# Kernel optimization log

Hardware: AMD Instinct MI355X
Metric: run time of the kernel (lower is better)

The kernel has to match this reference:

```python
import jax, jax.numpy as jnp
import numpy as np

C = 128  # n_filters; input channels must equal n_filters due to residual


def setup_inputs() -> dict:
    key = jax.random.key(0)
    kx, kw = jax.random.split(key)
    x = jax.random.normal(kx, (8, 64, 512, C), dtype=jnp.float32)
    # 1x1 conv, no bias == dense over channel axis: [C, 2C]
    W_qkv = jax.random.normal(kw, (C, 2 * C), dtype=jnp.float32) * (1.0 / np.sqrt(C))
    return {"x": x, "W_qkv": W_qkv}


def reference(x, W_qkv):
    # qkv: [B,H,W,2C]; split -> qk [B,H,W,C] -> q,k [B,H,W,C/2]; v [B,H,W,C]
    qkv = jnp.einsum('bhwc,cd->bhwd', x, W_qkv)
    half = C // 2
    q = qkv[..., :half]
    k = qkv[..., half:C]
    v = qkv[..., C:]
    # scores over the W (time) axis; NOTE: original applies no 1/sqrt(d) scaling
    scores = jnp.einsum('bhqc,bhkc->bhqk', q, k)  # [B,H,W,W]
    w = jax.nn.softmax(scores, axis=-1)
    y = jnp.einsum('bhqk,bhkc->bhqc', w, v)  # [B,H,W,C]
    y = x + y  # with_skip_connection=True
    return (y, w)
```

## Files before the change

### kernel.cpp

```cpp
#include <hip/hip_runtime.h>
#include <hip/hip_bf16.h>

typedef short s16x8 __attribute__((ext_vector_type(8)));
typedef float f32x4 __attribute__((ext_vector_type(4)));

#define MFMA_BF16(a,b,c) __builtin_amdgcn_mfma_f32_16x16x32_bf16((a),(b),(c),0,0,0)

static __device__ __forceinline__ unsigned short f2bf(float f){
  unsigned u = __builtin_bit_cast(unsigned, f);
  u += 0x7fffu + ((u >> 16) & 1u);
  return (unsigned short)(u >> 16);
}
static __device__ __forceinline__ float bf2f(unsigned short h){
  unsigned u = ((unsigned)h) << 16;
  return __builtin_bit_cast(float, u);
}
static __device__ __forceinline__ int swzi(int row, int col, int lw){
  const int chunk = (col >> 3) ^ ((row ^ (row >> 3)) & 7);
  return row*lw + (chunk << 3) + (col & 7);
}

__global__ __launch_bounds__(128) void k0_wt(const float* __restrict__ W,
                                             unsigned short* __restrict__ wtH,
                                             unsigned short* __restrict__ wtL){
  const int n = blockIdx.x;
  const int c = threadIdx.x;
  const float v = W[(size_t)c*256 + n];
  const unsigned short h = f2bf(v);
  wtH[n*128 + c] = h;
  wtL[n*128 + c] = f2bf(v - bf2f(h));
}

__global__ __launch_bounds__(512,2) void k1_qkv(const float* __restrict__ x,
    const unsigned short* __restrict__ wtH, const unsigned short* __restrict__ wtL,
    unsigned short* __restrict__ qh, unsigned short* __restrict__ ql,
    unsigned short* __restrict__ kh, unsigned short* __restrict__ kl,
    unsigned short* __restrict__ vT){
  __shared__ unsigned short xh[16384], xl[16384];
  const int t = threadIdx.x;
  const int lane = t & 63, wid = t >> 6;
  const int li = lane & 15, g = lane >> 4;
  const int m0 = blockIdx.x * 128;
  const int wm = wid >> 2, wn = wid & 3;

  {
    const int row = t >> 2, cb = (t & 3) * 32;
    const float* src = x + (size_t)(m0 + row)*128 + cb;
    #pragma unroll
    for (int gg = 0; gg < 4; ++gg){
      const float4 v0 = ((const float4*)src)[2*gg];
      const float4 v1 = ((const float4*)src)[2*gg + 1];
      const float vv[8] = {v0.x,v0.y,v0.z,v0.w,v1.x,v1.y,v1.z,v1.w};
      s16x8 h, l;
      #pragma unroll
      for (int j = 0; j < 8; ++j){
        const unsigned short hb = f2bf(vv[j]);
        h[j] = (short)hb;
        l[j] = (short)f2bf(vv[j] - bf2f(hb));
      }
      const int idx = swzi(row, cb + 8*gg, 128);
      *(s16x8*)&xh[idx] = h;
      *(s16x8*)&xl[idx] = l;
    }
  }
  __syncthreads();

  {
    f32x4 acc[4][2] = {};
    #pragma unroll
    for (int ks = 0; ks < 4; ++ks){
      const int col = ks*32 + g*8;
      s16x8 ah[4], al[4];
      #pragma unroll
      for (int mi = 0; mi < 4; ++mi){
        const int idx = swzi(wm*64 + mi*16 + li, col, 128);
        ah[mi] = *(const s16x8*)&xh[idx];
        al[mi] = *(const s16x8*)&xl[idx];
      }
      #pragma unroll
      for (int ni = 0; ni < 2; ++ni){
        const size_t boff = (size_t)(wn*32 + ni*16 + li)*128 + col;
        const s16x8 bh = *(const s16x8*)(wtH + boff);
        const s16x8 bl = *(const s16x8*)(wtL + boff);
        #pragma unroll
        for (int mi = 0; mi < 4; ++mi){
          acc[mi][ni] = MFMA_BF16(bh, ah[mi], acc[mi][ni]);
          acc[mi][ni] = MFMA_BF16(bh, al[mi], acc[mi][ni]);
          acc[mi][ni] = MFMA_BF16(bl, ah[mi], acc[mi][ni]);
        }
      }
    }
    #pragma unroll
    for (int mi = 0; mi < 4; ++mi)
      #pragma unroll
      for (int ni = 0; ni < 2; ++ni){
        const int pos = m0 + wm*64 + mi*16 + li;
        const int och = wn*32 + ni*16 + g*4;
        ushort4 hv, lv;
        #pragma unroll
        for (int r = 0; r < 4; ++r){
          const float v = acc[mi][ni][r];
          const unsigned short hb = f2bf(v);
          ((unsigned short*)&hv)[r] = hb;
          ((unsigned short*)&lv)[r] = f2bf(v - bf2f(hb));
        }
        const size_t off = (size_t)pos*64 + (och & 63);
        if (wn < 2){ *(ushort4*)&qh[off] = hv; *(ushort4*)&ql[off] = lv; }
        else       { *(ushort4*)&kh[off] = hv; *(ushort4*)&kl[off] = lv; }
      }
  }

  {
    f32x4 acc[4][2] = {};
    #pragma unroll
    for (int ks = 0; ks < 4; ++ks){
      const int col = ks*32 + g*8;
      s16x8 ah[4], al[4];
      #pragma unroll
      for (int mi = 0; mi < 4; ++mi){
        const int idx = swzi(wm*64 + mi*16 + li, col, 128);
        ah[mi] = *(const s16x8*)&xh[idx];
        al[mi] = *(const s16x8*)&xl[idx];
      }
      #pragma unroll
      for (int ni = 0; ni < 2; ++ni){
        const size_t boff = (size_t)(128 + wn*32 + ni*16 + li)*128 + col;
        const s16x8 bh = *(const s16x8*)(wtH + boff);
        const s16x8 bl = *(const s16x8*)(wtL + boff);
        #pragma unroll
        for (int mi = 0; mi < 4; ++mi){
          acc[mi][ni] = MFMA_BF16(ah[mi], bh, acc[mi][ni]);
          acc[mi][ni] = MFMA_BF16(ah[mi], bl, acc[mi][ni]);
          acc[mi][ni] = MFMA_BF16(al[mi], bh, acc[mi][ni]);
        }
      }
    }
    #pragma unroll
    for (int mi = 0; mi < 4; ++mi)
      #pragma unroll
      for (int ni = 0; ni < 2; ++ni){
        const int growb = m0 + wm*64 + mi*16 + g*4;
        const int ch = wn*32 + ni*16 + li;
        const int head = growb >> 9, posb = growb & 511;
        ushort4 pv;
        #pragma unroll
        for (int r = 0; r < 4; ++r)
          ((unsigned short*)&pv)[r] = f2bf(acc[mi][ni][r]);
        *(ushort4*)&vT[((size_t)head << 16) + ch*512 + posb] = pv;
      }
  }
}

__global__ __launch_bounds__(256,4) void k2_attn(
    const unsigned short* __restrict__ qh, const unsigned short* __restrict__ ql,
    const unsigned short* __restrict__ kh, const unsigned short* __restrict__ kl,
    const unsigned short* __restrict__ vT, const float* __restrict__ x,
    float* __restrict__ y, float* __restrict__ wout){
  __shared__ unsigned short wlds[16384];
  __shared__ float redm[128], reds[128];

  const int t = threadIdx.x;
  const int lane = t & 63, wid = t >> 6;
  const int li = lane & 15, g = lane >> 4;
  const int bi = blockIdx.x;
  const int head = (bi & 7) + 8 * (bi >> 7);
  const int qt = (bi >> 3) & 15;
  const size_t hbase = (size_t)head * 512;
  const int q0 = qt * 32;
  const int kbase = wid * 128;

  f32x4 acc[2][8] = {};
  #pragma unroll
  for (int ks = 0; ks < 2; ++ks){
    const int col = ks*32 + g*8;
    s16x8 ah[2], al[2];
    #pragma unroll
    for (int mi = 0; mi < 2; ++mi){
      const size_t aoff = (hbase + q0 + mi*16 + li)*64 + col;
      ah[mi] = *(const s16x8*)(qh + aoff);
      al[mi] = *(const s16x8*)(ql + aoff);
    }
    #pragma unroll
    for (int ni = 0; ni < 8; ++ni){
      const size_t boff = (hbase + kbase + ni*16 + li)*64 + col;
      const s16x8 bh = *(const s16x8*)(kh + boff);
      const s16x8 bl = *(const s16x8*)(kl + boff);
      #pragma unroll
      for (int mi = 0; mi < 2; ++mi){
        acc[mi][ni] = MFMA_BF16(ah[mi], bh, acc[mi][ni]);
        acc[mi][ni] = MFMA_BF16(ah[mi], bl, acc[mi][ni]);
        acc[mi][ni] = MFMA_BF16(al[mi], bh, acc[mi][ni]);
      }
    }
  }

  #pragma unroll
  for (int mi = 0; mi < 2; ++mi)
    #pragma unroll
    for (int r = 0; r < 4; ++r){
      float m = acc[mi][0][r];
      #pragma unroll
      for (int ni = 1; ni < 8; ++ni) m = fmaxf(m, acc[mi][ni][r]);
      #pragma unroll
      for (int d = 1; d < 16; d <<= 1) m = fmaxf(m, __shfl_xor(m, d));
      float s = 0.f;
      #pragma unroll
      for (int ni = 0; ni < 8; ++ni) s += __expf(acc[mi][ni][r] - m);
      #pragma unroll
      for (int d = 1; d < 16; d <<= 1) s += __shfl_xor(s, d);
      if (li == 0){
        const int row = mi*16 + g*4 + r;
        redm[row*4 + wid] = m;
        reds[row*4 + wid] = s;
      }
    }
  __syncthreads();

  float Mrow[2][4], Irow[2][4];
  #pragma unroll
  for (int mi = 0; mi < 2; ++mi)
    #pragma unroll
    for (int r = 0; r < 4; ++r){
      const int row = mi*16 + g*4 + r;
      const float4 mv = *(const float4*)&redm[row*4];
      const float4 sv = *(const float4*)&reds[row*4];
      const float M = fmaxf(fmaxf(mv.x, mv.y), fmaxf(mv.z, mv.w));
      const float S = sv.x*__expf(mv.x - M) + sv.y*__expf(mv.y - M)
                    + sv.z*__expf(mv.z - M) + sv.w*__expf(mv.w - M);
      Mrow[mi][r] = M;
      Irow[mi][r] = 1.0f / S;
    }

  #pragma unroll
  for (int mi = 0; mi < 2; ++mi)
    #pragma unroll
    for (int ni = 0; ni < 8; ++ni)
      #pragma unroll
      for (int r = 0; r < 4; ++r){
        const int row = mi*16 + g*4 + r;
        const int col = kbase + ni*16 + li;
        const float wv = __expf(acc[mi][ni][r] - Mrow[mi][r]) * Irow[mi][r];
        __builtin_nontemporal_store(wv, &wout[(hbase + q0 + row)*512 + col]);
        wlds[swzi(row, col, 512)] = f2bf(wv);
      }
  __syncthreads();

  const int c0 = wid * 32;
  f32x4 yacc[2][2] = {};
  #pragma unroll
  for (int kt = 0; kt < 16; ++kt){
    const int kp0 = kt*32 + g*8;
    s16x8 aw[2], vb[2];
    #pragma unroll
    for (int mi = 0; mi < 2; ++mi)
      aw[mi] = *(const s16x8*)&wlds[swzi(mi*16 + li, kp0, 512)];
    #pragma unroll
    for (int ci = 0; ci < 2; ++ci)
      vb[ci] = *(const s16x8*)&vT[((size_t)head << 16) + (size_t)(c0 + ci*16 + li)*512 + kp0];
    #pragma unroll
    for (int mi = 0; mi < 2; ++mi)
      #pragma unroll
      for (int ci = 0; ci < 2; ++ci)
        yacc[mi][ci] = MFMA_BF16(aw[mi], vb[ci], yacc[mi][ci]);
  }

  #pragma unroll
  for (int mi = 0; mi < 2; ++mi)
    #pragma unroll
    for (int ci = 0; ci < 2; ++ci)
      #pragma unroll
      for (int r = 0; r < 4; ++r){
        const int row = mi*16 + g*4 + r;
        const size_t idx = (hbase + q0 + row)*128 + c0 + ci*16 + li;
        const float xv = __builtin_nontemporal_load(&x[idx]);
        __builtin_nontemporal_store(xv + yacc[mi][ci][r], &y[idx]);
      }
}

extern "C" void kernel_launch(void* const* d_in, const int* in_sizes, int n_in,
                              void* d_out, int out_size, void* d_ws, size_t ws_size,
                              hipStream_t stream){
  (void)in_sizes; (void)n_in; (void)out_size; (void)ws_size;
  const float* x = (const float*)d_in[0];
  const float* W = (const float*)d_in[1];
  float* y    = (float*)d_out;
  float* wout = y + (size_t)33554432;

  char* ws = (char*)d_ws;
  unsigned short* qh  = (unsigned short*)(ws);
  unsigned short* ql  = (unsigned short*)(ws +  33554432ull);
  unsigned short* kh  = (unsigned short*)(ws +  67108864ull);
  unsigned short* kl  = (unsigned short*)(ws + 100663296ull);
  unsigned short* vT  = (unsigned short*)(ws + 134217728ull);
  unsigned short* wtH = (unsigned short*)(ws + 201326592ull);
  unsigned short* wtL = (unsigned short*)(ws + 201392128ull);

  hipLaunchKernelGGL(k0_wt,   dim3(256),  dim3(128), 0, stream, W, wtH, wtL);
  hipLaunchKernelGGL(k1_qkv,  dim3(2048), dim3(512), 0, stream, x, wtH, wtL,
                     qh, ql, kh, kl, vT);
  hipLaunchKernelGGL(k2_attn, dim3(8192), dim3(256), 0, stream,
                     qh, ql, kh, kl, vT, x, y, wout);
}
```

Before: 514.9 us.

## Restructure attention kernel into two-pass flash-style streaming with LDS-staged K tiles

Rewrites the attention kernel so each block handles 64 query rows, with one wave per 16 rows. It streams K in 64-key tiles through double-buffered LDS, first computing the row max and sum online, then recomputing the scores to write the normalized weights and accumulate W·V per tile. This replaces per-wave global K loads and the full 32x512 LDS weight buffer, cutting K traffic and LDS footprint and halving the block count. The cost is computing QK^T twice and doing strided global V loads inside the loop. The weight and y stores are now vectorized, normal rather than nontemporal stores.

```diff
diff --git a/kernel.cpp b/kernel.cpp
--- a/kernel.cpp
+++ b/kernel.cpp
@@ -156,125 +156,135 @@
     const unsigned short* __restrict__ kh, const unsigned short* __restrict__ kl,
     const unsigned short* __restrict__ vT, const float* __restrict__ x,
     float* __restrict__ y, float* __restrict__ wout){
-  __shared__ unsigned short wlds[16384];
-  __shared__ float redm[128], reds[128];
+  __shared__ unsigned short kth[2][4096], ktl[2][4096];
+  __shared__ unsigned short wtile[4096];
 
   const int t = threadIdx.x;
   const int lane = t & 63, wid = t >> 6;
   const int li = lane & 15, g = lane >> 4;
   const int bi = blockIdx.x;
-  const int head = (bi & 7) + 8 * (bi >> 7);
-  const int qt = (bi >> 3) & 15;
+  const int head = (bi & 7) + 8 * (bi >> 6);
+  const int qt = (bi >> 3) & 7;
   const size_t hbase = (size_t)head * 512;
-  const int q0 = qt * 32;
-  const int kbase = wid * 128;
-
-  f32x4 acc[2][8] = {};
+  const int qrow = qt*64 + wid*16 + li;
+
+  s16x8 qbh[2], qbl[2];
   #pragma unroll
   for (int ks = 0; ks < 2; ++ks){
-    const int col = ks*32 + g*8;
-    s16x8 ah[2], al[2];
-    #pragma unroll
-    for (int mi = 0; mi < 2; ++mi){
-      const size_t aoff = (hbase + q0 + mi*16 + li)*64 + col;
-      ah[mi] = *(const s16x8*)(qh + aoff);
-      al[mi] = *(const s16x8*)(ql + aoff);
-    }
-    #pragma unroll
-    for (int ni = 0; ni < 8; ++ni){
-      const size_t boff = (hbase + kbase + ni*16 + li)*64 + col;
-      const s16x8 bh = *(const s16x8*)(kh + boff);
-      const s16x8 bl = *(const s16x8*)(kl + boff);
-      #pragma unroll
-      for (int mi = 0; mi < 2; ++mi){
-        acc[mi][ni] = MFMA_BF16(ah[mi], bh, acc[mi][ni]);
-        acc[mi][ni] = MFMA_BF16(ah[mi], bl, acc[mi][ni]);
-        acc[mi][ni] = MFMA_BF16(al[mi], bh, acc[mi][ni]);
-      }
-    }
-  }
-
+    const size_t off = (hbase + qrow)*64 + ks*32 + g*8;
+    qbh[ks] = *(const s16x8*)(qh + off);
+    qbl[ks] = *(const s16x8*)(ql + off);
+  }
+
+  int srow[2], soff[2];
   #pragma unroll
-  for (int mi = 0; mi < 2; ++mi)
-    #pragma unroll
-    for (int r = 0; r < 4; ++r){
-      float m = acc[mi][0][r];
-      #pragma unroll
-      for (int ni = 1; ni < 8; ++ni) m = fmaxf(m, acc[mi][ni][r]);
-      #pragma unroll
-      for (int d = 1; d < 16; d <<= 1) m = fmaxf(m, __shfl_xor(m, d));
-      float s = 0.f;
-      #pragma unroll
-      for (int ni = 0; ni < 8; ++ni) s += __expf(acc[mi][ni][r] - m);
-      #pragma unroll
-      for (int d = 1; d < 16; d <<= 1) s += __shfl_xor(s, d);
-      if (li == 0){
-        const int row = mi*16 + g*4 + r;
-        redm[row*4 + wid] = m;
-        reds[row*4 + wid] = s;
-      }
-    }
+  for (int i = 0; i < 2; ++i){
+    const int gi = t + i*256;
+    const int row = gi >> 3, cs = gi & 7;
+    const int c = cs ^ ((row ^ (row >> 3)) & 7);
+    srow[i] = row; soff[i] = c*8;
+  }
+
+#define LOADT(kt) { \
+    _Pragma("unroll") for (int i = 0; i < 2; ++i){ \
+      const size_t sb = (hbase + (size_t)(kt)*64 + srow[i])*64 + soff[i]; \
+      ph[i] = *(const s16x8*)(kh + sb); \
+      pl[i] = *(const s16x8*)(kl + sb); } }
+#define WRITET(buf) { \
+    _Pragma("unroll") for (int i = 0; i < 2; ++i){ \
+      *(s16x8*)&kth[buf][(t + i*256)*8] = ph[i]; \
+      *(s16x8*)&ktl[buf][(t + i*256)*8] = pl[i]; } }
+#define QKT(buf, a) { \
+    _Pragma("unroll") for (int ks = 0; ks < 2; ++ks){ \
+      const int col = ks*32 + g*8; \
+      _Pragma("unroll") for (int ni = 0; ni < 4; ++ni){ \
+        const int idx = swzi(ni*16 + li, col, 64); \
+        const s16x8 ah = *(const s16x8*)&kth[buf][idx]; \
+        const s16x8 al = *(const s16x8*)&ktl[buf][idx]; \
+        a[ni] = MFMA_BF16(ah, qbh[ks], a[ni]); \
+        a[ni] = MFMA_BF16(al, qbh[ks], a[ni]); \
+        a[ni] = MFMA_BF16(ah, qbl[ks], a[ni]); } } }
+
+  s16x8 ph[2], pl[2];
+  float m = -3.0e38f, s = 0.f;
+
+  LOADT(0);
+  for (int kt = 0; kt < 8; ++kt){
+    WRITET(kt & 1);
+    __syncthreads();
+    if (kt < 7) LOADT(kt + 1);
+    f32x4 a[4] = {};
+    QKT(kt & 1, a);
+    float tm = a[0][0];
+    #pragma unroll
+    for (int ni = 0; ni < 4; ++ni)
+      #pragma unroll
+      for (int r = 0; r < 4; ++r) tm = fmaxf(tm, a[ni][r]);
+    tm = fmaxf(tm, __shfl_xor(tm, 16));
+    tm = fmaxf(tm, __shfl_xor(tm, 32));
+    const float mn = fmaxf(m, tm);
+    float ts = 0.f;
+    #pragma unroll
+    for (int ni = 0; ni < 4; ++ni)
+      #pragma unroll
+      for (int r = 0; r < 4; ++r) ts += __expf(a[ni][r] - mn);
+    ts += __shfl_xor(ts, 16);
+    ts += __shfl_xor(ts, 32);
+    s = s * __expf(m - mn) + ts;
+    m = mn;
+  }
+  const float invS = 1.0f / s;
   __syncthreads();
 
-  float Mrow[2][4], Irow[2][4];
+  f32x4 yacc[8] = {};
+  LOADT(0);
+  for (int kt = 0; kt < 8; ++kt){
+    WRITET(kt & 1);
+    __syncthreads();
+    if (kt < 7) LOADT(kt + 1);
+    f32x4 a[4] = {};
+    QKT(kt & 1, a);
+
+    float* wrow = wout + (hbase + qrow)*512 + kt*64;
+    #pragma unroll
+    for (int ni = 0; ni < 4; ++ni){
+      f32x4 wv; ushort4 pv;
+      #pragma unroll
+      for (int r = 0; r < 4; ++r){
+        const float v = __expf(a[ni][r] - m) * invS;
+        wv[r] = v;
+        ((unsigned short*)&pv)[r] = f2bf(v);
+      }
+      *(f32x4*)&wrow[ni*16 + g*4] = wv;
+      *(ushort4*)&wtile[swzi(wid*16 + li, ni*16 + g*4, 64)] = pv;
+    }
+
+    #pragma unroll
+    for (int ks = 0; ks < 2; ++ks){
+      const s16x8 aw = *(const s16x8*)&wtile[swzi(wid*16 + li, ks*32 + g*8, 64)];
+      const size_t vbase = ((size_t)head << 16) + (size_t)li*512 + kt*64 + ks*32 + g*8;
+      #pragma unroll
+      for (int ci = 0; ci < 8; ++ci){
+        const s16x8 vb = *(const s16x8*)&vT[vbase + (size_t)ci*8192];
+        yacc[ci] = MFMA_BF16(vb, aw, yacc[ci]);
+      }
+    }
+  }
+
   #pragma unroll
-  for (int mi = 0; mi < 2; ++mi)
-    #pragma unroll
-    for (int r = 0; r < 4; ++r){
-      const int row = mi*16 + g*4 + r;
-      const float4 mv = *(const float4*)&redm[row*4];
-      const float4 sv = *(const float4*)&reds[row*4];
-      const float M = fmaxf(fmaxf(mv.x, mv.y), fmaxf(mv.z, mv.w));
-      const float S = sv.x*__expf(mv.x - M) + sv.y*__expf(mv.y - M)
-                    + sv.z*__expf(mv.z - M) + sv.w*__expf(mv.w - M);
-      Mrow[mi][r] = M;
-      Irow[mi][r] = 1.0f / S;
-    }
-
-  #pragma unroll
-  for (int mi = 0; mi < 2; ++mi)
-    #pragma unroll
-    for (int ni = 0; ni < 8; ++ni)
-      #pragma unroll
-      for (int r = 0; r < 4; ++r){
-        const int row = mi*16 + g*4 + r;
-        const int col = kbase + ni*16 + li;
-        const float wv = __expf(acc[mi][ni][r] - Mrow[mi][r]) * Irow[mi][r];
-        __builtin_nontemporal_store(wv, &wout[(hbase + q0 + row)*512 + col]);
-        wlds[swzi(row, col, 512)] = f2bf(wv);
-      }
-  __syncthreads();
-
-  const int c0 = wid * 32;
-  f32x4 yacc[2][2] = {};
-  #pragma unroll
-  for (int kt = 0; kt < 16; ++kt){
-    const int kp0 = kt*32 + g*8;
-    s16x8 aw[2], vb[2];
-    #pragma unroll
-    for (int mi = 0; mi < 2; ++mi)
-      aw[mi] = *(const s16x8*)&wlds[swzi(mi*16 + li, kp0, 512)];
-    #pragma unroll
-    for (int ci = 0; ci < 2; ++ci)
-      vb[ci] = *(const s16x8*)&vT[((size_t)head << 16) + (size_t)(c0 + ci*16 + li)*512 + kp0];
-    #pragma unroll
-    for (int mi = 0; mi < 2; ++mi)
-      #pragma unroll
-      for (int ci = 0; ci < 2; ++ci)
-        yacc[mi][ci] = MFMA_BF16(aw[mi], vb[ci], yacc[mi][ci]);
-  }
-
-  #pragma unroll
-  for (int mi = 0; mi < 2; ++mi)
-    #pragma unroll
-    for (int ci = 0; ci < 2; ++ci)
-      #pragma unroll
-      for (int r = 0; r < 4; ++r){
-        const int row = mi*16 + g*4 + r;
-        const size_t idx = (hbase + q0 + row)*128 + c0 + ci*16 + li;
-        const float xv = __builtin_nontemporal_load(&x[idx]);
-        __builtin_nontemporal_store(xv + yacc[mi][ci][r], &y[idx]);
-      }
+  for (int ci = 0; ci < 8; ++ci){
+    const size_t idx = (hbase + qrow)*128 + ci*16 + g*4;
+    const f32x4 xv = __builtin_nontemporal_load((const f32x4*)&x[idx]);
+    f32x4 ov;
+    ov[0] = xv[0] + yacc[ci][0];
+    ov[1] = xv[1] + yacc[ci][1];
+    ov[2] = xv[2] + yacc[ci][2];
+    ov[3] = xv[3] + yacc[ci][3];
+    *(f32x4*)&y[idx] = ov;
+  }
+#undef LOADT
+#undef WRITET
+#undef QKT
 }
 
 extern "C" void kernel_launch(void* const* d_in, const int* in_sizes, int n_in,
@@ -298,6 +308,6 @@
   hipLaunchKernelGGL(k0_wt,   dim3(256),  dim3(128), 0, stream, W, wtH, wtL);
   hipLaunchKernelGGL(k1_qkv,  dim3(2048), dim3(512), 0, stream, x, wtH, wtL,
                      qh, ql, kh, kl, vT);
-  hipLaunchKernelGGL(k2_attn, dim3(8192), dim3(256), 0, stream,
+  hipLaunchKernelGGL(k2_attn, dim3(4096), dim3(256), 0, stream,
                      qh, ql, kh, kl, vT, x, y, wout);
 }
```

Measured after the change: 621.6 us. 1.21x slower.
